# Kernel tuning notes

Hardware: AMD Instinct MI355X
Metric: run time of the kernel (lower is better)

The kernel has to match this reference:

```python
import jax, jax.numpy as jnp
import numpy as np

SOBEL_X = jnp.array([[-1., 0., 1.], [-2., 0., 2.], [-1., 0., 1.]], dtype=jnp.float32).reshape(1, 1, 3, 3)
SOBEL_Y = jnp.array([[-1., -2., -1.], [0., 0., 0.], [1., 2., 1.]], dtype=jnp.float32).reshape(1, 1, 3, 3)
KERNEL_MASK = jnp.ones((1, 1, 3, 3), dtype=jnp.float32)


def _conv(x, k):
    # x: (N,1,H,W), k: (1,1,3,3), SAME padding (matches torch padding=1)
    return jax.lax.conv_general_dilated(
        x, k, window_strides=(1, 1), padding='SAME',
        dimension_numbers=('NCHW', 'OIHW', 'NCHW'))


def setup_inputs() -> dict:
    key = jax.random.key(0)
    k1, k2, k3 = jax.random.split(key, 3)
    shape = (2, 6, 512, 512, 8)  # (B, T, H, W, F)
    prediction = jax.random.normal(k1, shape, dtype=jnp.float32)
    target = jax.random.normal(k2, shape, dtype=jnp.float32)
    mask = jax.random.randint(k3, shape, 0, 2, dtype=jnp.int32)
    return {"prediction": prediction, "target": target, "mask": mask}


def reference(prediction, target, mask):
    B, T, H, W, F = prediction.shape
    # (B,T,H,W,F) -> (B*T*F, 1, H, W)
    def to_nchw(x):
        return x.transpose(0, 1, 4, 2, 3).reshape(B * T * F, 1, H, W)

    mask_r = to_nchw(mask.astype(jnp.float32))
    pred_r = to_nchw(prediction)
    tgt_r = to_nchw(target)

    valid = (_conv(mask_r, KERNEL_MASK) == 9.0).astype(prediction.dtype)

    gx_p = _conv(pred_r, SOBEL_X) * valid
    gy_p = _conv(pred_r, SOBEL_Y) * valid
    gx_t = _conv(tgt_r, SOBEL_X) * valid
    gy_t = _conv(tgt_r, SOBEL_Y) * valid

    # mode == 'l1'
    loss = jnp.abs(gx_p - gx_t) + jnp.abs(gy_p - gy_t)
    # (B*T*F,1,H,W) -> (B,T,H,W,F)
    return loss.reshape(B, T, F, H, W).transpose(0, 1, 3, 4, 2)
```

## Files before the change

### kernel.cpp

```cpp
#include <hip/hip_runtime.h>


constexpr int H = 512;
constexpr int W = 512;
constexpr int F = 8;
constexpr int IMAGES = 12;
constexpr int TH = 16;
constexpr int TWP = 32;
constexpr int SR = TH + 2;
constexpr int SP = TWP + 2;
constexpr int SU = SP * 2;
constexpr int TILES_PER_IMG = (H / TH) * (W / TWP);

__global__ __launch_bounds__(256) void sobel_loss_kernel(
    const float* __restrict__ pred,
    const float* __restrict__ tgt,
    const int*   __restrict__ mask,
    float*       __restrict__ out)
{
    __shared__ float4   sd[SR * SU];
    __shared__ unsigned sm[SR * SP];

    const int tid = threadIdx.x;
    const int img  = blockIdx.x >> 9;
    const int tile = blockIdx.x & 511;
    const int h0 = (tile >> 4) << 4;
    const int w0 = (tile & 15) << 5;
    const size_t ibase = (size_t)img * (H * W * F);

#pragma unroll
    for (int it = 0; it < 5; ++it) {
        const int s = tid + it * 256;
        if (s < SR * SU) {
            const int row = s / SU;
            const int u   = s - row * SU;
            const int gh  = h0 - 1 + row;
            const int gp  = w0 - 1 + (u >> 1);
            const int q   = u & 1;
            const int ghc = min(max(gh, 0), H - 1);
            const int gpc = min(max(gp, 0), W - 1);
            const size_t off = ibase + ((size_t)ghc * W + gpc) * F + q * 4;
            const float4 p = *(const float4*)(pred + off);
            const float4 t = *(const float4*)(tgt + off);
            sd[s] = make_float4(p.x - t.x, p.y - t.y, p.z - t.z, p.w - t.w);
        }
    }

#pragma unroll
    for (int it = 0; it < 3; ++it) {
        const int s = tid + it * 256;
        if (s < SR * SP) {
            const int row = s / SP;
            const int px  = s - row * SP;
            const int gh  = h0 - 1 + row;
            const int gp  = w0 - 1 + px;
            unsigned b = 0u;
            if (gh >= 0 && gh < H && gp >= 0 && gp < W) {
                const int* mp = mask + ibase + ((size_t)gh * W + gp) * F;
                const int4 m0 = *(const int4*)mp;
                const int4 m1 = *(const int4*)(mp + 4);
                b = (unsigned)(m0.x | (m0.y << 1) | (m0.z << 2) | (m0.w << 3) |
                               (m1.x << 4) | (m1.y << 5) | (m1.z << 6) | (m1.w << 7));
            }
            sm[s] = b;
        }
    }

    __syncthreads();

#pragma unroll
    for (int it = 0; it < 4; ++it) {
        const int o   = tid + it * 256;
        const int row = o >> 6;
        const int u   = o & 63;
        const int c   = u >> 1;
        const int q   = u & 1;

        float4 d[3][3];
        unsigned vm = 0xFFu;
#pragma unroll
        for (int dy = 0; dy < 3; ++dy) {
#pragma unroll
            for (int dx = 0; dx < 3; ++dx) {
                d[dy][dx] = sd[(row + dy) * SU + (c + dx) * 2 + q];
                vm &= sm[(row + dy) * SP + (c + dx)];
            }
        }
        const unsigned vq = vm >> (q * 4);

        float4 r;
#define SOBEL_COMP(comp, bit)                                                  \
        {                                                                      \
            float gx = (d[0][2].comp - d[0][0].comp)                           \
                     + 2.f * (d[1][2].comp - d[1][0].comp)                     \
                     + (d[2][2].comp - d[2][0].comp);                          \
            float gy = (d[2][0].comp - d[0][0].comp)                           \
                     + 2.f * (d[2][1].comp - d[0][1].comp)                     \
                     + (d[2][2].comp - d[0][2].comp);                          \
            r.comp = (vq & (1u << bit)) ? (fabsf(gx) + fabsf(gy)) : 0.f;       \
        }
        SOBEL_COMP(x, 0)
        SOBEL_COMP(y, 1)
        SOBEL_COMP(z, 2)
        SOBEL_COMP(w, 3)
#undef SOBEL_COMP

        const size_t off = ibase + ((size_t)(h0 + row) * W + (w0 + c)) * F + q * 4;
        *(float4*)(out + off) = r;
    }
}

extern "C" void kernel_launch(void* const* d_in, const int* in_sizes, int n_in,
                              void* d_out, int out_size, void* d_ws, size_t ws_size,
                              hipStream_t stream) {
    const float* pred = (const float*)d_in[0];
    const float* tgt  = (const float*)d_in[1];
    const int*   mask = (const int*)d_in[2];
    float*       out  = (float*)d_out;

    const int blocks = IMAGES * TILES_PER_IMG;
    sobel_loss_kernel<<<blocks, 256, 0, stream>>>(pred, tgt, mask, out);
}
```

Before: 303.6 us.

## Replace shared-memory tiles with register sliding-window Sobel using wave shuffles

Each wave now walks down an 8-row strip, 32 pixels wide, keeping three rows of horizontal Sobel partials in registers instead of staging an 18x34 tile in shared memory. Horizontal neighbours come from cross-lane shuffles, with edge lanes loading their halo pixel directly. The next row's pred, target and mask values are prefetched while the current row is computed, and outputs use nontemporal stores. The aim is to remove LDS traffic and the block barrier and to overlap loads with compute. In exchange it reads 10 input rows per 8 output rows, and edge lanes issue extra loads.

```diff
diff --git a/kernel.cpp b/kernel.cpp
--- a/kernel.cpp
+++ b/kernel.cpp
@@ -1,113 +1,128 @@
 #include <hip/hip_runtime.h>
 
 
-constexpr int H = 512;
-constexpr int W = 512;
-constexpr int F = 8;
+constexpr int H = 512, W = 512, F = 8;
 constexpr int IMAGES = 12;
-constexpr int TH = 16;
-constexpr int TWP = 32;
-constexpr int SR = TH + 2;
-constexpr int SP = TWP + 2;
-constexpr int SU = SP * 2;
-constexpr int TILES_PER_IMG = (H / TH) * (W / TWP);
+constexpr int SH = 8;
+constexpr int STRIPS = H / SH;
+constexpr int NIT = SH + 2;
 
-__global__ __launch_bounds__(256) void sobel_loss_kernel(
+typedef float f32x4 __attribute__((ext_vector_type(4)));
+
+__global__ __launch_bounds__(256, 4) void sobel_loss_kernel(
     const float* __restrict__ pred,
     const float* __restrict__ tgt,
     const int*   __restrict__ mask,
     float*       __restrict__ out)
 {
-    __shared__ float4   sd[SR * SU];
-    __shared__ unsigned sm[SR * SP];
+    const int tid  = threadIdx.x;
+    const int lane = tid & 63;
+    const int wid  = tid >> 6;
 
-    const int tid = threadIdx.x;
-    const int img  = blockIdx.x >> 9;
-    const int tile = blockIdx.x & 511;
-    const int h0 = (tile >> 4) << 4;
-    const int w0 = (tile & 15) << 5;
-    const size_t ibase = (size_t)img * (H * W * F);
+    const int bid   = blockIdx.x;
+    const int img   = bid >> 8;
+    const int rest  = bid & 255;
+    const int quad  = rest & 3;
+    const int strip = rest >> 2;
+    const int h0    = strip * SH;
 
-#pragma unroll
-    for (int it = 0; it < 5; ++it) {
-        const int s = tid + it * 256;
-        if (s < SR * SU) {
-            const int row = s / SU;
-            const int u   = s - row * SU;
-            const int gh  = h0 - 1 + row;
-            const int gp  = w0 - 1 + (u >> 1);
-            const int q   = u & 1;
-            const int ghc = min(max(gh, 0), H - 1);
-            const int gpc = min(max(gp, 0), W - 1);
-            const size_t off = ibase + ((size_t)ghc * W + gpc) * F + q * 4;
-            const float4 p = *(const float4*)(pred + off);
-            const float4 t = *(const float4*)(tgt + off);
-            sd[s] = make_float4(p.x - t.x, p.y - t.y, p.z - t.z, p.w - t.w);
-        }
+    const int p = lane >> 1;
+    const int q = lane & 1;
+    const int w = (quad * 4 + wid) * 32 + p;
+
+    const size_t ibase = (size_t)img * ((size_t)H * W * F);
+    const int voff = w * F + q * 4;
+    const bool eL = (p == 0);
+    const bool eR = (p == 31);
+    const bool edge = eL || eR;
+    const int wn   = eL ? (w > 0 ? w - 1 : 0) : (w < W - 1 ? w + 1 : W - 1);
+    const int eoff = wn * F + q * 4;
+    const bool win = (w > 0) & (w < W - 1);
+
+    float4 bp[2], bt[2]; int4 bm[2];
+    float4 bep[2], bet[2]; int4 bem[2];
+    float4 hx[3], hs[3]; unsigned hm[3];
+
+    bep[0] = bep[1] = bet[0] = bet[1] = make_float4(0.f, 0.f, 0.f, 0.f);
+    bem[0] = bem[1] = make_int4(0, 0, 0, 0);
+
+#define SUB4(a, b) make_float4((a).x - (b).x, (a).y - (b).y, (a).z - (b).z, (a).w - (b).w)
+
+#define PREFETCH(NB, HNX)                                                     \
+    {                                                                         \
+        const int hraw = (HNX);                                               \
+        const int hc = hraw < 0 ? 0 : (hraw >= H ? H - 1 : hraw);             \
+        const size_t ro = ibase + (size_t)hc * (W * F);                       \
+        bp[NB] = *(const float4*)(pred + ro + voff);                          \
+        bt[NB] = *(const float4*)(tgt  + ro + voff);                          \
+        bm[NB] = *(const int4*)(mask + ro + voff);                            \
+        if (edge) {                                                           \
+            bep[NB] = *(const float4*)(pred + ro + eoff);                     \
+            bet[NB] = *(const float4*)(tgt  + ro + eoff);                     \
+            bem[NB] = *(const int4*)(mask + ro + eoff);                       \
+        }                                                                     \
     }
 
-#pragma unroll
-    for (int it = 0; it < 3; ++it) {
-        const int s = tid + it * 256;
-        if (s < SR * SP) {
-            const int row = s / SP;
-            const int px  = s - row * SP;
-            const int gh  = h0 - 1 + row;
-            const int gp  = w0 - 1 + px;
-            unsigned b = 0u;
-            if (gh >= 0 && gh < H && gp >= 0 && gp < W) {
-                const int* mp = mask + ibase + ((size_t)gh * W + gp) * F;
-                const int4 m0 = *(const int4*)mp;
-                const int4 m1 = *(const int4*)(mp + 4);
-                b = (unsigned)(m0.x | (m0.y << 1) | (m0.z << 2) | (m0.w << 3) |
-                               (m1.x << 4) | (m1.y << 5) | (m1.z << 6) | (m1.w << 7));
-            }
-            sm[s] = b;
-        }
+    PREFETCH(0, h0 - 1)
+
+#define STEP(I)                                                               \
+    {                                                                         \
+        constexpr int i  = (I);                                               \
+        constexpr int cb = i & 1;                         \
+        constexpr int s2 = i % 3;           \
+        constexpr int s1 = (i + 2) % 3;                          \
+        constexpr int s0 = (i + 1) % 3;                          \
+        const int hin = h0 - 1 + i;                                           \
+        if constexpr (i < NIT - 1) PREFETCH(cb ^ 1, hin + 1)                  \
+        const float4 d  = SUB4(bp[cb], bt[cb]);                               \
+        const float4 ed = SUB4(bep[cb], bet[cb]);                             \
+        const unsigned m  = (unsigned)(bm[cb].x | (bm[cb].y << 1) |           \
+                                       (bm[cb].z << 2) | (bm[cb].w << 3));    \
+        const unsigned em = (unsigned)(bem[cb].x | (bem[cb].y << 1) |         \
+                                       (bem[cb].z << 2) | (bem[cb].w << 3));  \
+        float4 dl, dr;                                                        \
+        dl.x = __shfl_up(d.x, 2);   dl.y = __shfl_up(d.y, 2);                 \
+        dl.z = __shfl_up(d.z, 2);   dl.w = __shfl_up(d.w, 2);                 \
+        dr.x = __shfl_down(d.x, 2); dr.y = __shfl_down(d.y, 2);               \
+        dr.z = __shfl_down(d.z, 2); dr.w = __shfl_down(d.w, 2);               \
+        unsigned ml = (unsigned)__shfl_up((int)m, 2);                         \
+        unsigned mr = (unsigned)__shfl_down((int)m, 2);                       \
+        if (eL) { dl = ed; ml = em; }                                         \
+        if (eR) { dr = ed; mr = em; }                                         \
+        hx[s2] = SUB4(dr, dl);                                                \
+        hs[s2] = make_float4(dl.x + 2.f * d.x + dr.x,                         \
+                             dl.y + 2.f * d.y + dr.y,                         \
+                             dl.z + 2.f * d.z + dr.z,                         \
+                             dl.w + 2.f * d.w + dr.w);                        \
+        hm[s2] = ml & m & mr;                                                 \
+        if constexpr (i >= 2) {                                               \
+            const int r = hin - 1;                 \
+            unsigned vm = hm[0] & hm[1] & hm[2];                              \
+            if (!win || r == 0 || r == H - 1) vm = 0u;                        \
+            f32x4 o;                                                          \
+            { const float gx = hx[s0].x + 2.f * hx[s1].x + hx[s2].x;          \
+              const float gy = hs[s2].x - hs[s0].x;                           \
+              o.x = (vm & 1u) ? (fabsf(gx) + fabsf(gy)) : 0.f; }              \
+            { const float gx = hx[s0].y + 2.f * hx[s1].y + hx[s2].y;          \
+              const float gy = hs[s2].y - hs[s0].y;                           \
+              o.y = (vm & 2u) ? (fabsf(gx) + fabsf(gy)) : 0.f; }              \
+            { const float gx = hx[s0].z + 2.f * hx[s1].z + hx[s2].z;          \
+              const float gy = hs[s2].z - hs[s0].z;                           \
+              o.z = (vm & 4u) ? (fabsf(gx) + fabsf(gy)) : 0.f; }              \
+            { const float gx = hx[s0].w + 2.f * hx[s1].w + hx[s2].w;          \
+              const float gy = hs[s2].w - hs[s0].w;                           \
+              o.w = (vm & 8u) ? (fabsf(gx) + fabsf(gy)) : 0.f; }              \
+            __builtin_nontemporal_store(o,                                    \
+                (f32x4*)(out + ibase + (size_t)r * (W * F) + voff));          \
+        }                                                                     \
     }
 
-    __syncthreads();
+    STEP(0) STEP(1) STEP(2) STEP(3) STEP(4)
+    STEP(5) STEP(6) STEP(7) STEP(8) STEP(9)
 
-#pragma unroll
-    for (int it = 0; it < 4; ++it) {
-        const int o   = tid + it * 256;
-        const int row = o >> 6;
-        const int u   = o & 63;
-        const int c   = u >> 1;
-        const int q   = u & 1;
-
-        float4 d[3][3];
-        unsigned vm = 0xFFu;
-#pragma unroll
-        for (int dy = 0; dy < 3; ++dy) {
-#pragma unroll
-            for (int dx = 0; dx < 3; ++dx) {
-                d[dy][dx] = sd[(row + dy) * SU + (c + dx) * 2 + q];
-                vm &= sm[(row + dy) * SP + (c + dx)];
-            }
-        }
-        const unsigned vq = vm >> (q * 4);
-
-        float4 r;
-#define SOBEL_COMP(comp, bit)                                                  \
-        {                                                                      \
-            float gx = (d[0][2].comp - d[0][0].comp)                           \
-                     + 2.f * (d[1][2].comp - d[1][0].comp)                     \
-                     + (d[2][2].comp - d[2][0].comp);                          \
-            float gy = (d[2][0].comp - d[0][0].comp)                           \
-                     + 2.f * (d[2][1].comp - d[0][1].comp)                     \
-                     + (d[2][2].comp - d[0][2].comp);                          \
-            r.comp = (vq & (1u << bit)) ? (fabsf(gx) + fabsf(gy)) : 0.f;       \
-        }
-        SOBEL_COMP(x, 0)
-        SOBEL_COMP(y, 1)
-        SOBEL_COMP(z, 2)
-        SOBEL_COMP(w, 3)
-#undef SOBEL_COMP
-
-        const size_t off = ibase + ((size_t)(h0 + row) * W + (w0 + c)) * F + q * 4;
-        *(float4*)(out + off) = r;
-    }
+#undef STEP
+#undef PREFETCH
+#undef SUB4
 }
 
 extern "C" void kernel_launch(void* const* d_in, const int* in_sizes, int n_in,
@@ -118,6 +133,6 @@
     const int*   mask = (const int*)d_in[2];
     float*       out  = (float*)d_out;
 
-    const int blocks = IMAGES * TILES_PER_IMG;
+    const int blocks = IMAGES * 4 * STRIPS;
     sobel_loss_kernel<<<blocks, 256, 0, stream>>>(pred, tgt, mask, out);
 }
```

Measured after the change: 314.9 us. +3.7%, slower.

## Retile into wide row strips with per-wave row loads and nontemporal stores

Applied to the files above, without the earlier changes.

Replaces the 16x32 pixel tiles with 6-row by 128-pixel strips processed by 512-thread blocks, where each wave loads one halo row with contiguous, coalesced float4 loads and only a few lanes fetch the edge pixels. The mask is packed per half-pixel into 16-bit shared entries, and block IDs are swizzled across groups of eight. Output is written with nontemporal stores. The aim is to cut halo overhead, remove the integer div/mod indexing, and improve load coalescing, at the cost of more halo rows relative to output rows (8 loaded for 6 output) and a partial strip at the image bottom.

```diff
diff --git a/kernel.cpp b/kernel.cpp
--- a/kernel.cpp
+++ b/kernel.cpp
@@ -1,112 +1,144 @@
 #include <hip/hip_runtime.h>
 
 
-constexpr int H = 512;
-constexpr int W = 512;
-constexpr int F = 8;
+constexpr int H = 512, W = 512, F = 8;
 constexpr int IMAGES = 12;
-constexpr int TH = 16;
-constexpr int TWP = 32;
-constexpr int SR = TH + 2;
-constexpr int SP = TWP + 2;
-constexpr int SU = SP * 2;
-constexpr int TILES_PER_IMG = (H / TH) * (W / TWP);
+constexpr int SPAN  = 128;
+constexpr int NSPAN = W / SPAN;
+constexpr int ORWS  = 6;
+constexpr int SRWS  = 8;
+constexpr int STRIPS = (H + ORWS - 1) / ORWS;
+constexpr int NB = IMAGES * NSPAN * STRIPS;
+constexpr int UROW = 2 * SPAN + 4;
 
-__global__ __launch_bounds__(256) void sobel_loss_kernel(
+typedef float f32x4 __attribute__((ext_vector_type(4)));
+
+__global__ __launch_bounds__(512) void sobel_loss_kernel(
     const float* __restrict__ pred,
     const float* __restrict__ tgt,
     const int*   __restrict__ mask,
     float*       __restrict__ out)
 {
-    __shared__ float4   sd[SR * SU];
-    __shared__ unsigned sm[SR * SP];
+    __shared__ float4         dls[SRWS * UROW];
+    __shared__ unsigned short mls[SRWS * UROW];
 
-    const int tid = threadIdx.x;
-    const int img  = blockIdx.x >> 9;
-    const int tile = blockIdx.x & 511;
-    const int h0 = (tile >> 4) << 4;
-    const int w0 = (tile & 15) << 5;
-    const size_t ibase = (size_t)img * (H * W * F);
+    const int tid  = threadIdx.x;
+    const int l    = tid & 63;
+    const int wv   = tid >> 6;
 
+    const int b0  = blockIdx.x;
+    const int bid = (b0 & 7) * (NB >> 3) + (b0 >> 3);
+
+    const int img   = bid / (NSPAN * STRIPS);
+    const int rest  = bid - img * (NSPAN * STRIPS);
+    const int span  = rest / STRIPS;
+    const int strip = rest - span * STRIPS;
+
+    const int r0 = strip * ORWS;
+    const int w0 = span * SPAN;
+
+    const size_t ibase = (size_t)img * ((size_t)H * W * F);
+
+    {
+        const int gr  = r0 - 1 + wv;
+        const int grc = gr < 0 ? 0 : (gr >= H ? H - 1 : gr);
+        const bool rv = (gr >= 0) & (gr < H);
+        const size_t rowf = ibase + (size_t)grc * (W * F) + (size_t)w0 * F;
+
+        float4 P[4], T[4]; int4 M[4];
 #pragma unroll
-    for (int it = 0; it < 5; ++it) {
-        const int s = tid + it * 256;
-        if (s < SR * SU) {
-            const int row = s / SU;
-            const int u   = s - row * SU;
-            const int gh  = h0 - 1 + row;
-            const int gp  = w0 - 1 + (u >> 1);
-            const int q   = u & 1;
-            const int ghc = min(max(gh, 0), H - 1);
-            const int gpc = min(max(gp, 0), W - 1);
-            const size_t off = ibase + ((size_t)ghc * W + gpc) * F + q * 4;
-            const float4 p = *(const float4*)(pred + off);
-            const float4 t = *(const float4*)(tgt + off);
-            sd[s] = make_float4(p.x - t.x, p.y - t.y, p.z - t.z, p.w - t.w);
+        for (int k = 0; k < 4; ++k) {
+            const size_t o = rowf + (size_t)k * 256 + l * 4;
+            P[k] = *(const float4*)(pred + o);
+            T[k] = *(const float4*)(tgt  + o);
+            M[k] = *(const int4*)(mask + o);
         }
-    }
 
+        float4 EP = make_float4(0.f,0.f,0.f,0.f), ET = EP;
+        int4   EM = make_int4(0,0,0,0);
+        const bool left = (l < 2);
+        const int  qe   = l & 1;
+        const int  pxg  = left ? (w0 - 1) : (w0 + SPAN);
+        const bool ib   = (pxg >= 0) & (pxg < W);
+        if (l < 4) {
+            const int pxc = ib ? pxg : 0;
+            const size_t o = ibase + (size_t)grc * (W * F) + (size_t)pxc * F + qe * 4;
+            EP = *(const float4*)(pred + o);
+            ET = *(const float4*)(tgt  + o);
+            EM = *(const int4*)(mask + o);
+        }
+
+        float4* drow = dls + wv * UROW;
+        unsigned short* mrow = mls + wv * UROW;
 #pragma unroll
-    for (int it = 0; it < 3; ++it) {
-        const int s = tid + it * 256;
-        if (s < SR * SP) {
-            const int row = s / SP;
-            const int px  = s - row * SP;
-            const int gh  = h0 - 1 + row;
-            const int gp  = w0 - 1 + px;
-            unsigned b = 0u;
-            if (gh >= 0 && gh < H && gp >= 0 && gp < W) {
-                const int* mp = mask + ibase + ((size_t)gh * W + gp) * F;
-                const int4 m0 = *(const int4*)mp;
-                const int4 m1 = *(const int4*)(mp + 4);
-                b = (unsigned)(m0.x | (m0.y << 1) | (m0.z << 2) | (m0.w << 3) |
-                               (m1.x << 4) | (m1.y << 5) | (m1.z << 6) | (m1.w << 7));
-            }
-            sm[s] = b;
+        for (int k = 0; k < 4; ++k) {
+            const int u = 2 + k * 64 + l;
+            drow[u] = make_float4(P[k].x - T[k].x, P[k].y - T[k].y,
+                                  P[k].z - T[k].z, P[k].w - T[k].w);
+            const unsigned bits = (unsigned)(M[k].x | (M[k].y << 1) |
+                                             (M[k].z << 2) | (M[k].w << 3));
+            mrow[u] = (unsigned short)(rv ? bits : 0u);
+        }
+        if (l < 4) {
+            const int u = left ? qe : (2 + 2 * SPAN + qe);
+            drow[u] = make_float4(EP.x - ET.x, EP.y - ET.y,
+                                  EP.z - ET.z, EP.w - ET.w);
+            const unsigned bits = (unsigned)(EM.x | (EM.y << 1) |
+                                             (EM.z << 2) | (EM.w << 3));
+            mrow[u] = (unsigned short)((rv && ib) ? bits : 0u);
         }
     }
 
     __syncthreads();
 
 #pragma unroll
-    for (int it = 0; it < 4; ++it) {
-        const int o   = tid + it * 256;
-        const int row = o >> 6;
-        const int u   = o & 63;
-        const int c   = u >> 1;
-        const int q   = u & 1;
+    for (int pass = 0; pass < 3; ++pass) {
+        const int ot = tid + pass * 512;
+        const int ol = ot >> 8;
+        const int uo = ot & 255;
+        const int ro = r0 + ol;
+        if (ro < H) {
+            const int bc = (ol + 1) * UROW + 2 + uo;
 
-        float4 d[3][3];
-        unsigned vm = 0xFFu;
-#pragma unroll
-        for (int dy = 0; dy < 3; ++dy) {
-#pragma unroll
-            for (int dx = 0; dx < 3; ++dx) {
-                d[dy][dx] = sd[(row + dy) * SU + (c + dx) * 2 + q];
-                vm &= sm[(row + dy) * SP + (c + dx)];
+            const float4 a0 = dls[bc - UROW - 2];
+            const float4 a1 = dls[bc - UROW];
+            const float4 a2 = dls[bc - UROW + 2];
+            const unsigned mA = (unsigned)mls[bc - UROW - 2] &
+                                (unsigned)mls[bc - UROW] &
+                                (unsigned)mls[bc - UROW + 2];
+            const float4 b0r = dls[bc - 2];
+            const float4 b1r = dls[bc];
+            const float4 b2r = dls[bc + 2];
+            const unsigned mB = (unsigned)mls[bc - 2] &
+                                (unsigned)mls[bc] &
+                                (unsigned)mls[bc + 2];
+            const float4 c0 = dls[bc + UROW - 2];
+            const float4 c1 = dls[bc + UROW];
+            const float4 c2 = dls[bc + UROW + 2];
+            const unsigned mC = (unsigned)mls[bc + UROW - 2] &
+                                (unsigned)mls[bc + UROW] &
+                                (unsigned)mls[bc + UROW + 2];
+
+            const unsigned vm = mA & mB & mC;
+
+            f32x4 o;
+#define COMP(cc, bit)                                                          \
+            {                                                                  \
+                const float hx0 = a2.cc - a0.cc;                               \
+                const float hx1 = b2r.cc - b0r.cc;                             \
+                const float hx2 = c2.cc - c0.cc;                               \
+                const float hs0 = a0.cc + 2.f * a1.cc + a2.cc;                 \
+                const float hs2 = c0.cc + 2.f * c1.cc + c2.cc;                 \
+                const float gx = hx0 + 2.f * hx1 + hx2;                        \
+                const float gy = hs2 - hs0;                                    \
+                o.cc = (vm & (1u << bit)) ? (fabsf(gx) + fabsf(gy)) : 0.f;     \
             }
+            COMP(x, 0) COMP(y, 1) COMP(z, 2) COMP(w, 3)
+#undef COMP
+
+            float* const op = out + ibase + ((size_t)ro * W + w0) * F + uo * 4;
+            __builtin_nontemporal_store(o, (f32x4*)op);
         }
-        const unsigned vq = vm >> (q * 4);
-
-        float4 r;
-#define SOBEL_COMP(comp, bit)                                                  \
-        {                                                                      \
-            float gx = (d[0][2].comp - d[0][0].comp)                           \
-                     + 2.f * (d[1][2].comp - d[1][0].comp)                     \
-                     + (d[2][2].comp - d[2][0].comp);                          \
-            float gy = (d[2][0].comp - d[0][0].comp)                           \
-                     + 2.f * (d[2][1].comp - d[0][1].comp)                     \
-                     + (d[2][2].comp - d[0][2].comp);                          \
-            r.comp = (vq & (1u << bit)) ? (fabsf(gx) + fabsf(gy)) : 0.f;       \
-        }
-        SOBEL_COMP(x, 0)
-        SOBEL_COMP(y, 1)
-        SOBEL_COMP(z, 2)
-        SOBEL_COMP(w, 3)
-#undef SOBEL_COMP
-
-        const size_t off = ibase + ((size_t)(h0 + row) * W + (w0 + c)) * F + q * 4;
-        *(float4*)(out + off) = r;
     }
 }
 
@@ -118,6 +150,5 @@
     const int*   mask = (const int*)d_in[2];
     float*       out  = (float*)d_out;
 
-    const int blocks = IMAGES * TILES_PER_IMG;
-    sobel_loss_kernel<<<blocks, 256, 0, stream>>>(pred, tgt, mask, out);
+    sobel_loss_kernel<<<NB, 512, 0, stream>>>(pred, tgt, mask, out);
 }
```

New measurement: 314.2 us. 1.03x slower.
